# Kernel optimization log

Measured on AMD Instinct MI355X. Metric: run time of the kernel, lower is better.

Reference implementation:

```python
import jax, jax.numpy as jnp
import numpy as np
import math

L_MAX = 4
R_BINS = 16
R_MAX = 8.0
VOXEL = 0.5


def _precompute_basis():
    # grid: n = floor(2*r_max/voxel)+1 points per axis, g = n^3
    n = int(math.floor(2 * R_MAX / VOXEL)) + 1
    xs = np.linspace(-R_MAX, R_MAX, n)
    X, Y, Z = np.meshgrid(xs, xs, xs, indexing='ij')
    xyz = np.stack([X, Y, Z], -1).reshape(-1, 3)
    r = np.maximum(np.sqrt((xyz ** 2).sum(-1)), 1e-12)
    ct = np.clip(xyz[:, 2] / r, -1.0, 1.0)           # cos(theta)
    phi = np.arctan2(xyz[:, 1], xyz[:, 0])
    G = xyz.shape[0]
    L = L_MAX
    st = np.sqrt(np.maximum(0.0, 1.0 - ct ** 2))     # sin(theta)
    # associated Legendre P_l^m(cos theta) with Condon-Shortley phase
    P = np.zeros((L + 1, L + 1, G))
    P[0, 0] = 1.0
    for m in range(1, L + 1):
        P[m, m] = -(2 * m - 1) * st * P[m - 1, m - 1]
    for m in range(L):
        P[m + 1, m] = (2 * m + 1) * ct * P[m, m]
    for m in range(L + 1):
        for l in range(m + 2, L + 1):
            P[l, m] = ((2 * l - 1) * ct * P[l - 1, m] - (l + m - 1) * P[l - 2, m]) / (l - m)
    # real spherical harmonics, 'component' normalization (= sqrt(4pi) * orthonormal real SH),
    # packed centered on the m axis: column index L_MAX + m  (mirrors split_Y_by_l_centered)
    Mmax = 2 * L + 1
    Ylmg = np.zeros((L + 1, Mmax, G))
    for l in range(L + 1):
        for m in range(0, l + 1):
            norm = math.sqrt((2 * l + 1) * math.factorial(l - m) / math.factorial(l + m))
            base = norm * P[l, m]
            if m == 0:
                Ylmg[l, L] = base
            else:
                Ylmg[l, L + m] = math.sqrt(2.0) * base * np.cos(m * phi)
                Ylmg[l, L - m] = math.sqrt(2.0) * base * np.sin(m * phi)
    # radial Gaussian RBF (make_radial_rbf), transposed to [R, G]
    edges = np.linspace(0.0, R_MAX, R_BINS + 1)
    centers = 0.5 * (edges[:-1] + edges[1:])
    sigma = (edges[1] - edges[0]) * 0.5
    Rbf = np.exp(-0.5 * ((r[:, None] - centers) / (sigma + 1e-12)) ** 2).T
    return Ylmg.astype(np.float32), Rbf.astype(np.float32)


def setup_inputs() -> dict:
    key = jax.random.key(0)
    Y_lmg, Rbf = _precompute_basis()               # [5,9,35937], [16,35937]
    coeffs = jax.random.normal(key, (2, 32, 4, L_MAX + 1, 2 * L_MAX + 1, R_BINS), dtype=jnp.float32)
    return {"coeffs": coeffs, "Y_lmg": jnp.asarray(Y_lmg), "Rbf": jnp.asarray(Rbf)}


def reference(coeffs, Y_lmg, Rbf):
    # fused equivalent of torch.einsum('bnclmr,lmg,rg->bncg', coeffs, Y_lmg, Rbf)
    # contraction order chosen to avoid the huge (b,n,c,r,g) intermediate:
    basis = jnp.einsum('lmg,rg->lmrg', Y_lmg, Rbf)          # [5,9,16,G] ~103MB
    density = jnp.einsum('bnclmr,lmrg->bncg', coeffs, basis)
    return density.astype(jnp.float16)
```

## Files before the change

### kernel.cpp

```cpp
#include <hip/hip_runtime.h>


#define G_TOTAL 35937
#define N_ROWS  256

typedef __attribute__((ext_vector_type(8))) short bf16x8;
typedef __attribute__((ext_vector_type(16))) float f32x16;

__constant__ int c_lmFlat[25] = {4, 12,13,14, 20,21,22,23,24,
                                 28,29,30,31,32,33,34,
                                 36,37,38,39,40,41,42,43,44};

__global__ __launch_bounds__(512, 4) void sh_fused(
        const float* __restrict__ coeffs,
        const float* __restrict__ Y,
        const float* __restrict__ Rb,
        float* __restrict__ out) {
    __shared__ uint4 Alds[50 * 64];
    const int tx = threadIdx.x;
    const int l  = tx & 63;
    const int w  = tx >> 6;
    const int cl = l & 31;
    const int kg = l >> 5;

    const int bY = blockIdx.y;
    const int g  = blockIdx.x * 256 + w * 32 + cl;
    const int gc = g < G_TOTAL ? g : G_TOTAL - 1;

#pragma unroll
    for (int i = 0; i < 4; ++i) {
        int c = tx + i * 512;
        if (c < 1600) {
            int ks   = c >> 6;
            int rowl = c & 63;
            int mtl  = rowl >> 5;
            int r32  = rowl & 31;
            const float4* src = (const float4*)(coeffs + (bY * 64 + rowl) * 720
                                                + c_lmFlat[ks] * 16);
            float4 f0 = src[0], f1 = src[1], f2 = src[2], f3 = src[3];
            unsigned u0, u1, u2, u3, u4, u5, u6, u7;
            asm("v_cvt_pk_bf16_f32 %0, %1, %2" : "=v"(u0) : "v"(f0.x), "v"(f0.y));
            asm("v_cvt_pk_bf16_f32 %0, %1, %2" : "=v"(u1) : "v"(f0.z), "v"(f0.w));
            asm("v_cvt_pk_bf16_f32 %0, %1, %2" : "=v"(u2) : "v"(f1.x), "v"(f1.y));
            asm("v_cvt_pk_bf16_f32 %0, %1, %2" : "=v"(u3) : "v"(f1.z), "v"(f1.w));
            asm("v_cvt_pk_bf16_f32 %0, %1, %2" : "=v"(u4) : "v"(f2.x), "v"(f2.y));
            asm("v_cvt_pk_bf16_f32 %0, %1, %2" : "=v"(u5) : "v"(f2.z), "v"(f2.w));
            asm("v_cvt_pk_bf16_f32 %0, %1, %2" : "=v"(u6) : "v"(f3.x), "v"(f3.y));
            asm("v_cvt_pk_bf16_f32 %0, %1, %2" : "=v"(u7) : "v"(f3.z), "v"(f3.w));
            int fbase = (ks * 2 + mtl) * 64;
            Alds[fbase + r32]      = make_uint4(u0, u1, u2, u3);
            Alds[fbase + 32 + r32] = make_uint4(u4, u5, u6, u7);
        }
    }

    constexpr int lmFlat[25] = {4, 12,13,14, 20,21,22,23,24,
                                28,29,30,31,32,33,34,
                                36,37,38,39,40,41,42,43,44};
    float YA[25];
#pragma unroll
    for (int i = 0; i < 25; ++i) YA[i] = Y[lmFlat[i] * G_TOTAL + gc];

    float RA[8];
#pragma unroll
    for (int j = 0; j < 8; ++j) RA[j] = Rb[(kg * 8 + j) * G_TOTAL + gc];

    f32x16 acc0, acc1;
#pragma unroll
    for (int q = 0; q < 16; ++q) { acc0[q] = 0.0f; acc1[q] = 0.0f; }

    __syncthreads();

    const bf16x8* __restrict__ Al = (const bf16x8*)Alds;
#pragma unroll
    for (int ks = 0; ks < 25; ++ks) {
        const float y = YA[ks];
        union { unsigned int u[4]; bf16x8 v; } fb;
#pragma unroll
        for (int p = 0; p < 4; ++p) {
            float lo = y * RA[2 * p];
            float hi = y * RA[2 * p + 1];
            unsigned r;
            asm("v_cvt_pk_bf16_f32 %0, %1, %2" : "=v"(r) : "v"(lo), "v"(hi));
            fb.u[p] = r;
        }
        bf16x8 a0 = Al[(ks * 2 + 0) * 64 + l];
        bf16x8 a1 = Al[(ks * 2 + 1) * 64 + l];
        acc0 = __builtin_amdgcn_mfma_f32_32x32x16_bf16(a0, fb.v, acc0, 0, 0, 0);
        acc1 = __builtin_amdgcn_mfma_f32_32x32x16_bf16(a1, fb.v, acc1, 0, 0, 0);
    }

    if (g < G_TOTAL) {
        const int rb0 = (2 * bY)     * 32 + 4 * kg;
        const int rb1 = (2 * bY + 1) * 32 + 4 * kg;
#pragma unroll
        for (int reg = 0; reg < 16; ++reg) {
            int ro = (reg & 3) + 8 * (reg >> 2);
            out[(rb0 + ro) * G_TOTAL + g] = acc0[reg];
            out[(rb1 + ro) * G_TOTAL + g] = acc1[reg];
        }
    }
}

extern "C" void kernel_launch(void* const* d_in, const int* in_sizes, int n_in,
                              void* d_out, int out_size, void* d_ws, size_t ws_size,
                              hipStream_t stream) {
    const float *pC = nullptr, *pY = nullptr, *pR = nullptr;
    if (n_in >= 3) {
        for (int i = 0; i < 3; ++i) {
            if      (in_sizes[i] == 256 * 720)    pC = (const float*)d_in[i];
            else if (in_sizes[i] == 45 * G_TOTAL) pY = (const float*)d_in[i];
            else if (in_sizes[i] == 16 * G_TOTAL) pR = (const float*)d_in[i];
        }
    }
    if (!pC || !pY || !pR) {
        pC = (const float*)d_in[0];
        pY = (const float*)d_in[1];
        pR = (const float*)d_in[2];
    }

    float* out = (float*)d_out;

    dim3 grid(141, 4);
    sh_fused<<<grid, 512, 0, stream>>>(pC, pY, pR, out);

    (void)d_ws; (void)ws_size; (void)out_size; (void)n_in;
}
```

Before: 24.70 us.

## Retile MFMA work so each wave shares one A fragment across two grid tiles

Each block now covers 32 output rows instead of 64, and each wave handles 64 grid points instead of 32. One LDS coefficient fragment is reused for two MFMAs with different B operands, and the block shrinks to 256 threads with twice as many blocks along y. This halves the LDS footprint and LDS reads per MFMA. In exchange, each thread builds two B fragments and holds twice the Y/Rbf registers, and Y/Rbf are reloaded by 8 row-blocks instead of 4.

```diff
diff --git a/kernel.cpp b/kernel.cpp
--- a/kernel.cpp
+++ b/kernel.cpp
@@ -11,31 +11,31 @@
                                  28,29,30,31,32,33,34,
                                  36,37,38,39,40,41,42,43,44};
 
-__global__ __launch_bounds__(512, 4) void sh_fused(
+__global__ __launch_bounds__(256, 3) void sh_fused(
         const float* __restrict__ coeffs,
         const float* __restrict__ Y,
         const float* __restrict__ Rb,
         float* __restrict__ out) {
-    __shared__ uint4 Alds[50 * 64];
+    __shared__ uint4 Alds[25 * 64];
     const int tx = threadIdx.x;
     const int l  = tx & 63;
     const int w  = tx >> 6;
     const int cl = l & 31;
     const int kg = l >> 5;
 
-    const int bY = blockIdx.y;
-    const int g  = blockIdx.x * 256 + w * 32 + cl;
-    const int gc = g < G_TOTAL ? g : G_TOTAL - 1;
+    const int mt = blockIdx.y;
+    const int g0 = blockIdx.x * 256 + w * 64 + cl;
+    const int g1 = g0 + 32;
+    const int gc0 = g0 < G_TOTAL ? g0 : G_TOTAL - 1;
+    const int gc1 = g1 < G_TOTAL ? g1 : G_TOTAL - 1;
 
 #pragma unroll
     for (int i = 0; i < 4; ++i) {
-        int c = tx + i * 512;
-        if (c < 1600) {
-            int ks   = c >> 6;
-            int rowl = c & 63;
-            int mtl  = rowl >> 5;
-            int r32  = rowl & 31;
-            const float4* src = (const float4*)(coeffs + (bY * 64 + rowl) * 720
+        int c = tx + i * 256;
+        if (c < 800) {
+            int ks  = c >> 5;
+            int r32 = c & 31;
+            const float4* src = (const float4*)(coeffs + (mt * 32 + r32) * 720
                                                 + c_lmFlat[ks] * 16);
             float4 f0 = src[0], f1 = src[1], f2 = src[2], f3 = src[3];
             unsigned u0, u1, u2, u3, u4, u5, u6, u7;
@@ -47,22 +47,26 @@
             asm("v_cvt_pk_bf16_f32 %0, %1, %2" : "=v"(u5) : "v"(f2.z), "v"(f2.w));
             asm("v_cvt_pk_bf16_f32 %0, %1, %2" : "=v"(u6) : "v"(f3.x), "v"(f3.y));
             asm("v_cvt_pk_bf16_f32 %0, %1, %2" : "=v"(u7) : "v"(f3.z), "v"(f3.w));
-            int fbase = (ks * 2 + mtl) * 64;
-            Alds[fbase + r32]      = make_uint4(u0, u1, u2, u3);
-            Alds[fbase + 32 + r32] = make_uint4(u4, u5, u6, u7);
+            Alds[ks * 64 + r32]      = make_uint4(u0, u1, u2, u3);
+            Alds[ks * 64 + 32 + r32] = make_uint4(u4, u5, u6, u7);
         }
     }
 
     constexpr int lmFlat[25] = {4, 12,13,14, 20,21,22,23,24,
                                 28,29,30,31,32,33,34,
                                 36,37,38,39,40,41,42,43,44};
-    float YA[25];
+    float YA[25], YB[25];
 #pragma unroll
-    for (int i = 0; i < 25; ++i) YA[i] = Y[lmFlat[i] * G_TOTAL + gc];
-
-    float RA[8];
+    for (int i = 0; i < 25; ++i) {
+        YA[i] = Y[lmFlat[i] * G_TOTAL + gc0];
+        YB[i] = Y[lmFlat[i] * G_TOTAL + gc1];
+    }
+    float RA[8], RB[8];
 #pragma unroll
-    for (int j = 0; j < 8; ++j) RA[j] = Rb[(kg * 8 + j) * G_TOTAL + gc];
+    for (int j = 0; j < 8; ++j) {
+        RA[j] = Rb[(kg * 8 + j) * G_TOTAL + gc0];
+        RB[j] = Rb[(kg * 8 + j) * G_TOTAL + gc1];
+    }
 
     f32x16 acc0, acc1;
 #pragma unroll
@@ -73,30 +77,37 @@
     const bf16x8* __restrict__ Al = (const bf16x8*)Alds;
 #pragma unroll
     for (int ks = 0; ks < 25; ++ks) {
-        const float y = YA[ks];
-        union { unsigned int u[4]; bf16x8 v; } fb;
+        const float y0 = YA[ks];
+        const float y1 = YB[ks];
+        union { unsigned int u[4]; bf16x8 v; } fb0, fb1;
 #pragma unroll
         for (int p = 0; p < 4; ++p) {
-            float lo = y * RA[2 * p];
-            float hi = y * RA[2 * p + 1];
-            unsigned r;
-            asm("v_cvt_pk_bf16_f32 %0, %1, %2" : "=v"(r) : "v"(lo), "v"(hi));
-            fb.u[p] = r;
+            float a_lo = y0 * RA[2 * p], a_hi = y0 * RA[2 * p + 1];
+            float b_lo = y1 * RB[2 * p], b_hi = y1 * RB[2 * p + 1];
+            unsigned ra, rb;
+            asm("v_cvt_pk_bf16_f32 %0, %1, %2" : "=v"(ra) : "v"(a_lo), "v"(a_hi));
+            asm("v_cvt_pk_bf16_f32 %0, %1, %2" : "=v"(rb) : "v"(b_lo), "v"(b_hi));
+            fb0.u[p] = ra;
+            fb1.u[p] = rb;
         }
-        bf16x8 a0 = Al[(ks * 2 + 0) * 64 + l];
-        bf16x8 a1 = Al[(ks * 2 + 1) * 64 + l];
-        acc0 = __builtin_amdgcn_mfma_f32_32x32x16_bf16(a0, fb.v, acc0, 0, 0, 0);
-        acc1 = __builtin_amdgcn_mfma_f32_32x32x16_bf16(a1, fb.v, acc1, 0, 0, 0);
+        bf16x8 a = Al[ks * 64 + l];
+        acc0 = __builtin_amdgcn_mfma_f32_32x32x16_bf16(a, fb0.v, acc0, 0, 0, 0);
+        acc1 = __builtin_amdgcn_mfma_f32_32x32x16_bf16(a, fb1.v, acc1, 0, 0, 0);
     }
 
-    if (g < G_TOTAL) {
-        const int rb0 = (2 * bY)     * 32 + 4 * kg;
-        const int rb1 = (2 * bY + 1) * 32 + 4 * kg;
+    const int rbase = mt * 32 + 4 * kg;
+    if (g0 < G_TOTAL) {
 #pragma unroll
         for (int reg = 0; reg < 16; ++reg) {
             int ro = (reg & 3) + 8 * (reg >> 2);
-            out[(rb0 + ro) * G_TOTAL + g] = acc0[reg];
-            out[(rb1 + ro) * G_TOTAL + g] = acc1[reg];
+            out[(rbase + ro) * G_TOTAL + g0] = acc0[reg];
+        }
+    }
+    if (g1 < G_TOTAL) {
+#pragma unroll
+        for (int reg = 0; reg < 16; ++reg) {
+            int ro = (reg & 3) + 8 * (reg >> 2);
+            out[(rbase + ro) * G_TOTAL + g1] = acc1[reg];
         }
     }
 }
@@ -120,8 +131,8 @@
 
     float* out = (float*)d_out;
 
-    dim3 grid(141, 4);
-    sh_fused<<<grid, 512, 0, stream>>>(pC, pY, pR, out);
+    dim3 grid(141, 8);
+    sh_fused<<<grid, 256, 0, stream>>>(pC, pY, pR, out);
 
     (void)d_ws; (void)ws_size; (void)out_size; (void)n_in;
 }
```

Result: slower. 25.34 us (+2.6%).
